# Performance work log

Measured on AMD Instinct MI355X. Metric: run time of the kernel, lower is better.

## Reference

```python
import jax, jax.numpy as jnp
import numpy as np


def _lstm(x, w_ih, w_hh, b_ih, b_hh):
    # x: [B, T, D]; w_ih: [4H, D]; w_hh: [4H, H]. PyTorch gate order: i, f, g, o.
    B, T, D = x.shape
    H = w_hh.shape[1]
    # Precompute input contributions for all timesteps: [B, T, 4H]
    xg = jnp.einsum('btd,gd->btg', x, w_ih) + b_ih + b_hh
    xg = jnp.transpose(xg, (1, 0, 2))  # [T, B, 4H]

    def step(carry, xt):
        h, c = carry
        gates = xt + h @ w_hh.T  # [B, 4H]
        i, f, g, o = jnp.split(gates, 4, axis=-1)
        i = jax.nn.sigmoid(i)
        f = jax.nn.sigmoid(f)
        g = jnp.tanh(g)
        o = jax.nn.sigmoid(o)
        c = f * c + i * g
        h = o * jnp.tanh(c)
        return (h, c), h

    h0 = jnp.zeros((B, H), dtype=x.dtype)
    c0 = jnp.zeros((B, H), dtype=x.dtype)
    (_, _), hs = jax.lax.scan(step, (h0, c0), xg)
    return jnp.transpose(hs, (1, 0, 2))  # [B, T, H]


def setup_inputs() -> dict:
    key = jax.random.key(0)
    ks = jax.random.split(key, 11)
    B, T, D, H1, H2, OUT = 2048, 128, 128, 128, 64, 64
    s1 = 1.0 / np.sqrt(H1)
    s2 = 1.0 / np.sqrt(H2)
    return {
        'x': jax.random.normal(ks[0], (B, T, D), dtype=jnp.float32),
        'w_ih1': jax.random.uniform(ks[1], (4 * H1, D), jnp.float32, -s1, s1),
        'w_hh1': jax.random.uniform(ks[2], (4 * H1, H1), jnp.float32, -s1, s1),
        'b_ih1': jax.random.uniform(ks[3], (4 * H1,), jnp.float32, -s1, s1),
        'b_hh1': jax.random.uniform(ks[4], (4 * H1,), jnp.float32, -s1, s1),
        'w_ih2': jax.random.uniform(ks[5], (4 * H2, H1), jnp.float32, -s2, s2),
        'w_hh2': jax.random.uniform(ks[6], (4 * H2, H2), jnp.float32, -s2, s2),
        'b_ih2': jax.random.uniform(ks[7], (4 * H2,), jnp.float32, -s2, s2),
        'b_hh2': jax.random.uniform(ks[8], (4 * H2,), jnp.float32, -s2, s2),
        'w_dense': jax.random.uniform(ks[9], (OUT, H2), jnp.float32, -s2, s2),
        'b_dense': jax.random.uniform(ks[10], (OUT,), jnp.float32, -s2, s2),
    }


def reference(x, w_ih1, w_hh1, b_ih1, b_hh1, w_ih2, w_hh2, b_ih2, b_hh2, w_dense, b_dense):
    # Dropout is identity in eval mode.
    h = _lstm(x, w_ih1, w_hh1, b_ih1, b_hh1)          # [B, T, H1]
    h = _lstm(h, w_ih2, w_hh2, b_ih2, b_hh2)          # [B, T, H2]
    last = h[:, -1, :]                                 # [B, H2]
    return jax.nn.relu(last @ w_dense.T + b_dense)     # [B, 64]
```

## Files before the change

kernel.cpp:

```cpp
#include <hip/hip_runtime.h>
#include <hip/hip_bf16.h>

#define BB  2048
#define TT  128
#define DD  128
#define HH1 128
#define GG1 512
#define HH2 64
#define GG2 256
#define OO  64

typedef __attribute__((ext_vector_type(8))) short  short8;
typedef __attribute__((ext_vector_type(4))) float  floatx4;

#define PIN(x) asm volatile("" : "+v"(x))

#define OFF_WHH1 0
#define OFF_WIH1 131072
#define OFF_WIH2 262144
#define OFF_WHH2 327680
#define OFF_B1   360448
#define OFF_B2   362496
#define OFF_XBF  524288
#define OFF_H1S  67633152

#define L2E      1.44269504088896340736f
#define TWO_L2E  2.88539008177792681472f

__device__ __forceinline__ short f2bf(float f) {
  unsigned u = __float_as_uint(f);
  unsigned r = (u + 0x7FFFu + ((u >> 16) & 1u)) >> 16;
  return (short)r;
}
__device__ __forceinline__ float exp2_f(float x) {
  float r; asm("v_exp_f32 %0, %1" : "=v"(r) : "v"(x)); return r;
}
__device__ __forceinline__ float sigm2(float y) {
  return __builtin_amdgcn_rcpf(1.0f + exp2_f(y));
}
__device__ __forceinline__ float tanh2(float y) {
  return fmaf(-2.0f, __builtin_amdgcn_rcpf(1.0f + exp2_f(y)), 1.0f);
}

__device__ __forceinline__ void lds_barrier() {
  asm volatile("s_waitcnt lgkmcnt(0)" ::: "memory");
  __builtin_amdgcn_s_barrier();
  asm volatile("" ::: "memory");
}

__global__ void k_prep(const float* __restrict__ wih1, const float* __restrict__ whh1,
                       const float* __restrict__ bih1, const float* __restrict__ bhh1,
                       const float* __restrict__ wih2, const float* __restrict__ whh2,
                       const float* __restrict__ bih2, const float* __restrict__ bhh2,
                       char* __restrict__ ws) {
  short* WHH1 = (short*)(ws + OFF_WHH1);
  short* WIH1 = (short*)(ws + OFF_WIH1);
  short* WIH2 = (short*)(ws + OFF_WIH2);
  short* WHH2 = (short*)(ws + OFF_WHH2);
  float* B1 = (float*)(ws + OFF_B1);
  float* B2 = (float*)(ws + OFF_B2);
  int idx = blockIdx.x * blockDim.x + threadIdx.x;
  int stride = gridDim.x * blockDim.x;
  const float SCI = -L2E, SCG = TWO_L2E;
  for (int i = idx; i < GG1 * DD; i += stride) {
    int g = (i >> 7) >> 7;
    float s = (g == 2) ? SCG : SCI;
    WIH1[i] = f2bf(wih1[i] * s); WHH1[i] = f2bf(whh1[i] * s);
  }
  for (int i = idx; i < GG2 * HH1; i += stride) {
    int g = (i >> 7) >> 6; float s = (g == 2) ? SCG : SCI;
    WIH2[i] = f2bf(wih2[i] * s);
  }
  for (int i = idx; i < GG2 * HH2; i += stride) {
    int g = (i >> 6) >> 6; float s = (g == 2) ? SCG : SCI;
    WHH2[i] = f2bf(whh2[i] * s);
  }
  for (int i = idx; i < GG1; i += stride) {
    float s = ((i >> 7) == 2) ? SCG : SCI;
    B1[i] = (bih1[i] + bhh1[i]) * s;
  }
  for (int i = idx; i < GG2; i += stride) {
    float s = ((i >> 6) == 2) ? SCG : SCI;
    B2[i] = (bih2[i] + bhh2[i]) * s;
  }
}

__global__ __launch_bounds__(256) void k_xcast(const float* __restrict__ x,
                                               short* __restrict__ xbf) {
  size_t i = ((size_t)blockIdx.x * 256 + threadIdx.x) * 8;
  float4 a = *(const float4*)&x[i];
  float4 b = *(const float4*)&x[i + 4];
  short8 o;
  o[0] = f2bf(a.x); o[1] = f2bf(a.y); o[2] = f2bf(a.z); o[3] = f2bf(a.w);
  o[4] = f2bf(b.x); o[5] = f2bf(b.y); o[6] = f2bf(b.z); o[7] = f2bf(b.w);
  *(short8*)&xbf[i] = o;
}

__global__ __launch_bounds__(512, 2) void k_rec1f(const char* __restrict__ ws,
                                                  short* __restrict__ h1s) {
  __shared__ short hbds[2][16 * 136];
  const short* WHH = (const short*)(ws + OFF_WHH1);
  const short* WIH = (const short*)(ws + OFF_WIH1);
  const short* XBF = (const short*)(ws + OFF_XBF);
  const float* B1 = (const float*)(ws + OFF_B1);
  const int lane = threadIdx.x & 63;
  const int wv = threadIdx.x >> 6;
  const int col = lane & 15, quad = lane >> 4;
  const int hc = wv * 16 + col;
  const int r0 = blockIdx.x * 8;

  short8 wh[4][4], wx[4][4];
#pragma unroll
  for (int gt = 0; gt < 4; ++gt)
#pragma unroll
    for (int kk = 0; kk < 4; ++kk) {
      wh[gt][kk] = *(const short8*)&WHH[(gt * 128 + hc) * HH1 + kk * 32 + quad * 8];
      wx[gt][kk] = *(const short8*)&WIH[(gt * 128 + hc) * DD + kk * 32 + quad * 8];
      PIN(wh[gt][kk]);
      PIN(wx[gt][kk]);
    }
  floatx4 BIASV[4];
#pragma unroll
  for (int gt = 0; gt < 4; ++gt) {
    float b = B1[gt * 128 + hc];
    BIASV[gt] = (floatx4){b, b, b, b};
    PIN(BIASV[gt]);
  }

  for (int i = threadIdx.x; i < 2 * 16 * 136; i += 512) ((short*)hbds)[i] = 0;

  const bool aload = (col < 8);
  const short* xbase = XBF + (size_t)(r0 + (col & 7)) * TT * DD;
  const short8 zz = {0, 0, 0, 0, 0, 0, 0, 0};
  short8 axA[4], axB[4];
  floatx4 accA[4], accB[4];

  {
    short8 ax0[4];
#pragma unroll
    for (int kk = 0; kk < 4; ++kk)
      ax0[kk] = aload ? *(const short8*)&xbase[kk * 32 + quad * 8] : zz;
#pragma unroll
    for (int gt = 0; gt < 4; ++gt)
      accA[gt] = __builtin_amdgcn_mfma_f32_16x16x32_bf16(ax0[0], wx[gt][0], BIASV[gt], 0, 0, 0);
#pragma unroll
    for (int kk = 1; kk < 4; ++kk)
#pragma unroll
      for (int gt = 0; gt < 4; ++gt)
        accA[gt] = __builtin_amdgcn_mfma_f32_16x16x32_bf16(ax0[kk], wx[gt][kk], accA[gt], 0, 0, 0);
  }
#pragma unroll
  for (int kk = 0; kk < 4; ++kk) {
    axA[kk] = aload ? *(const short8*)&xbase[DD + kk * 32 + quad * 8] : zz;
    axB[kk] = zz;
  }

  const int row0 = (quad & 1) * 4 + (quad >> 1) * 2;
  float c0 = 0.f, c1 = 0.f;
  __syncthreads();

  auto step = [&](int t, short* rbuf, short* wbuf, floatx4* A, floatx4* Bn,
                  short8* axC, short8* axP) {
    if (aload && t + 2 < TT) {
#pragma unroll
      for (int kk = 0; kk < 4; ++kk)
        axP[kk] = *(const short8*)&xbase[(t + 2) * DD + kk * 32 + quad * 8];
    }
    short8 ah[4];
#pragma unroll
    for (int kk = 0; kk < 4; ++kk)
      ah[kk] = *(const short8*)&rbuf[col * 136 + kk * 32 + quad * 8];
#pragma unroll
    for (int kk = 0; kk < 4; ++kk)
#pragma unroll
      for (int gt = 0; gt < 4; ++gt)
        A[gt] = __builtin_amdgcn_mfma_f32_16x16x32_bf16(ah[kk], wh[gt][kk], A[gt], 0, 0, 0);
#pragma unroll
    for (int gt = 0; gt < 4; ++gt)
      Bn[gt] = __builtin_amdgcn_mfma_f32_16x16x32_bf16(axC[0], wx[gt][0], BIASV[gt], 0, 0, 0);
#pragma unroll
    for (int kk = 1; kk < 4; ++kk)
#pragma unroll
      for (int gt = 0; gt < 4; ++gt)
        Bn[gt] = __builtin_amdgcn_mfma_f32_16x16x32_bf16(axC[kk], wx[gt][kk], Bn[gt], 0, 0, 0);

    float g0[4], g1[4];
#pragma unroll
    for (int gt = 0; gt < 4; ++gt) {
      float v2 = __shfl_xor(A[gt][2], 32);
      float v3 = __shfl_xor(A[gt][3], 32);
      g0[gt] = (quad < 2) ? A[gt][0] : v2;
      g1[gt] = (quad < 2) ? A[gt][1] : v3;
    }
    {
      float i0 = sigm2(g0[0]), f0 = sigm2(g0[1]), gg0 = tanh2(g0[2]), o0 = sigm2(g0[3]);
      c0 = fmaf(f0, c0, i0 * gg0);
      float hA = o0 * tanh2(c0 * TWO_L2E);
      float i1 = sigm2(g1[0]), f1 = sigm2(g1[1]), gg1 = tanh2(g1[2]), o1 = sigm2(g1[3]);
      c1 = fmaf(f1, c1, i1 * gg1);
      float hB = o1 * tanh2(c1 * TWO_L2E);
      short ha = f2bf(hA), hbv = f2bf(hB);
      wbuf[(row0)     * 136 + hc] = ha;
      wbuf[(row0 + 1) * 136 + hc] = hbv;
      h1s[((size_t)(r0 + row0)     * TT + t) * HH1 + hc] = ha;
      h1s[((size_t)(r0 + row0 + 1) * TT + t) * HH1 + hc] = hbv;
    }
    lds_barrier();
  };

  for (int t = 0; t < TT; t += 2) {
    step(t,     &hbds[0][0], &hbds[1][0], accA, accB, axA, axB);
    step(t + 1, &hbds[1][0], &hbds[0][0], accB, accA, axB, axA);
  }
}

__global__ __launch_bounds__(512, 2) void k_rec2w(const char* __restrict__ ws,
                                                  const short* __restrict__ h1s,
                                                  const float* __restrict__ wd,
                                                  const float* __restrict__ bd,
                                                  float* __restrict__ out) {
  __shared__ __align__(16) float xacc[2][256 * 20];
  __shared__ short hbuf[2][16 * 72];
  __shared__ float h2f[8 * HH2];
  const int lane = threadIdx.x & 63;
  const int wv = threadIdx.x >> 6;
  const int col = lane & 15, quad = lane >> 4;
  const int r0 = blockIdx.x * 8;

  for (int i = threadIdx.x; i < 2 * 256 * 20; i += 512) ((float*)xacc)[i] = 0.f;
  for (int i = threadIdx.x; i < 2 * 16 * 72; i += 512) ((short*)hbuf)[i] = 0;

  if (wv >= 4) {
    const short* WIH = (const short*)(ws + OFF_WIH2);
    const float* B2 = (const float*)(ws + OFF_B2);
    const int hcp = (wv - 4) * 16 + col;
    short8 wx[4][4];
#pragma unroll
    for (int gt = 0; gt < 4; ++gt)
#pragma unroll
      for (int kk = 0; kk < 4; ++kk) {
        wx[gt][kk] = *(const short8*)&WIH[(gt * 64 + hcp) * HH1 + kk * 32 + quad * 8];
        PIN(wx[gt][kk]);
      }
    floatx4 BIASV[4];
#pragma unroll
    for (int gt = 0; gt < 4; ++gt) {
      float b = B2[gt * 64 + hcp];
      BIASV[gt] = (floatx4){b, b, b, b};
      PIN(BIASV[gt]);
    }
    const bool aload = (col < 8);
    const short* h1base = h1s + (size_t)(r0 + (col & 7)) * TT * HH1;
    const short8 zz = {0, 0, 0, 0, 0, 0, 0, 0};
    short8 axA[4], axB[4];

    {
      short8 ax0[4];
#pragma unroll
      for (int kk = 0; kk < 4; ++kk)
        ax0[kk] = aload ? *(const short8*)&h1base[kk * 32 + quad * 8] : zz;
      floatx4 Bn[4];
#pragma unroll
      for (int gt = 0; gt < 4; ++gt)
        Bn[gt] = __builtin_amdgcn_mfma_f32_16x16x32_bf16(ax0[0], wx[gt][0], BIASV[gt], 0, 0, 0);
#pragma unroll
      for (int kk = 1; kk < 4; ++kk)
#pragma unroll
        for (int gt = 0; gt < 4; ++gt)
          Bn[gt] = __builtin_amdgcn_mfma_f32_16x16x32_bf16(ax0[kk], wx[gt][kk], Bn[gt], 0, 0, 0);
      if (quad < 2) {
#pragma unroll
        for (int gt = 0; gt < 4; ++gt)
          *(floatx4*)&xacc[0][(gt * 64 + hcp) * 20 + quad * 4] = Bn[gt];
      }
    }
#pragma unroll
    for (int kk = 0; kk < 4; ++kk) {
      axA[kk] = aload ? *(const short8*)&h1base[HH1 + kk * 32 + quad * 8] : zz;
      axB[kk] = zz;
    }
    __syncthreads();

    auto pstep = [&](int t, short8* axC, short8* axP) {
      if (t + 1 < TT) {
        floatx4 Bn[4];
#pragma unroll
        for (int gt = 0; gt < 4; ++gt)
          Bn[gt] = __builtin_amdgcn_mfma_f32_16x16x32_bf16(axC[0], wx[gt][0], BIASV[gt], 0, 0, 0);
#pragma unroll
        for (int kk = 1; kk < 4; ++kk)
#pragma unroll
          for (int gt = 0; gt < 4; ++gt)
            Bn[gt] = __builtin_amdgcn_mfma_f32_16x16x32_bf16(axC[kk], wx[gt][kk], Bn[gt], 0, 0, 0);
        if (quad < 2) {
#pragma unroll
          for (int gt = 0; gt < 4; ++gt)
            *(floatx4*)&xacc[(t + 1) & 1][(gt * 64 + hcp) * 20 + quad * 4] = Bn[gt];
        }
      }
      if (aload && t + 2 < TT) {
#pragma unroll
        for (int kk = 0; kk < 4; ++kk)
          axP[kk] = *(const short8*)&h1base[(t + 2) * HH1 + kk * 32 + quad * 8];
      }
      lds_barrier();
    };

    for (int t = 0; t < TT; t += 2) {
      pstep(t, axA, axB);
      pstep(t + 1, axB, axA);
    }

  } else {
    const short* WHH = (const short*)(ws + OFF_WHH2);
    const int hc = wv * 16 + col;
    short8 wh[4][2];
#pragma unroll
    for (int gt = 0; gt < 4; ++gt)
#pragma unroll
      for (int kk = 0; kk < 2; ++kk) {
        wh[gt][kk] = *(const short8*)&WHH[(gt * 64 + hc) * HH2 + kk * 32 + quad * 8];
        PIN(wh[gt][kk]);
      }
    const int row0 = (quad & 1) * 4 + (quad >> 1) * 2;
    float c0 = 0.f, c1 = 0.f;
    __syncthreads();

    auto cstep = [&](int t) {
      const int cur = t & 1;
      short8 ah[2];
#pragma unroll
      for (int kk = 0; kk < 2; ++kk)
        ah[kk] = *(const short8*)&hbuf[cur][col * 72 + kk * 32 + quad * 8];
      floatx4 A[4];
#pragma unroll
      for (int gt = 0; gt < 4; ++gt)
        A[gt] = *(const floatx4*)&xacc[cur][(gt * 64 + hc) * 20 + quad * 4];
#pragma unroll
      for (int kk = 0; kk < 2; ++kk)
#pragma unroll
        for (int gt = 0; gt < 4; ++gt)
          A[gt] = __builtin_amdgcn_mfma_f32_16x16x32_bf16(ah[kk], wh[gt][kk], A[gt], 0, 0, 0);

      float g0[4], g1[4];
#pragma unroll
      for (int gt = 0; gt < 4; ++gt) {
        float v2 = __shfl_xor(A[gt][2], 32);
        float v3 = __shfl_xor(A[gt][3], 32);
        g0[gt] = (quad < 2) ? A[gt][0] : v2;
        g1[gt] = (quad < 2) ? A[gt][1] : v3;
      }
      float i0 = sigm2(g0[0]), f0 = sigm2(g0[1]), gg0 = tanh2(g0[2]), o0 = sigm2(g0[3]);
      c0 = fmaf(f0, c0, i0 * gg0);
      float hA = o0 * tanh2(c0 * TWO_L2E);
      float i1 = sigm2(g1[0]), f1 = sigm2(g1[1]), gg1 = tanh2(g1[2]), o1 = sigm2(g1[3]);
      c1 = fmaf(f1, c1, i1 * gg1);
      float hB = o1 * tanh2(c1 * TWO_L2E);
      hbuf[cur ^ 1][(row0)     * 72 + hc] = f2bf(hA);
      hbuf[cur ^ 1][(row0 + 1) * 72 + hc] = f2bf(hB);
      if (t == TT - 1) {
        h2f[(row0)     * HH2 + hc] = hA;
        h2f[(row0 + 1) * HH2 + hc] = hB;
      }
      lds_barrier();
    };

    for (int t = 0; t < TT; ++t) cstep(t);
  }

  __syncthreads();

  {
    const int o = threadIdx.x & 63;
    const int r = threadIdx.x >> 6;
    float acc = bd[o];
    for (int k = 0; k < HH2; ++k)
      acc = fmaf(h2f[r * HH2 + k], wd[o * HH2 + k], acc);
    out[(size_t)(r0 + r) * OO + o] = fmaxf(acc, 0.f);
  }
}

extern "C" void kernel_launch(void* const* d_in, const int* in_sizes, int n_in,
                              void* d_out, int out_size, void* d_ws, size_t ws_size,
                              hipStream_t stream) {
  const float* x       = (const float*)d_in[0];
  const float* w_ih1   = (const float*)d_in[1];
  const float* w_hh1   = (const float*)d_in[2];
  const float* b_ih1   = (const float*)d_in[3];
  const float* b_hh1   = (const float*)d_in[4];
  const float* w_ih2   = (const float*)d_in[5];
  const float* w_hh2   = (const float*)d_in[6];
  const float* b_ih2   = (const float*)d_in[7];
  const float* b_hh2   = (const float*)d_in[8];
  const float* w_dense = (const float*)d_in[9];
  const float* b_dense = (const float*)d_in[10];
  char* ws = (char*)d_ws;
  short* xbf = (short*)(ws + OFF_XBF);
  short* h1s = (short*)(ws + OFF_H1S);
  float* out = (float*)d_out;

  hipLaunchKernelGGL(k_prep, dim3(256), dim3(256), 0, stream,
                     w_ih1, w_hh1, b_ih1, b_hh1, w_ih2, w_hh2, b_ih2, b_hh2, ws);
  hipLaunchKernelGGL(k_xcast, dim3((BB * TT * DD) / (256 * 8)), dim3(256), 0, stream, x, xbf);
  hipLaunchKernelGGL(k_rec1f, dim3(BB / 8), dim3(512), 0, stream, ws, h1s);
  hipLaunchKernelGGL(k_rec2w, dim3(BB / 8), dim3(512), 0, stream, ws, h1s, w_dense, b_dense, out);
}
```

Measured before the change: 414.4 us.

## Fuse x bf16 cast into layer-1 recurrence via LDS ring buffer

Removes the separate x-to-bf16 cast kernel. The layer-1 recurrent kernel now reads fp32 x directly, converts it with packed bf16 conversion, and stages it into a 4-deep LDS ring with register prefetch several timesteps ahead. This eliminates a full write and reread of the bf16 copy of x and one kernel launch. In exchange, the recurrent kernel does the conversion and the larger fp32 loads, and uses extra LDS.

```diff
diff --git a/kernel.cpp b/kernel.cpp
--- a/kernel.cpp
+++ b/kernel.cpp
@@ -21,7 +21,6 @@
 #define OFF_WHH2 327680
 #define OFF_B1   360448
 #define OFF_B2   362496
-#define OFF_XBF  524288
 #define OFF_H1S  67633152
 
 #define L2E      1.44269504088896340736f
@@ -40,6 +39,11 @@
 }
 __device__ __forceinline__ float tanh2(float y) {
   return fmaf(-2.0f, __builtin_amdgcn_rcpf(1.0f + exp2_f(y)), 1.0f);
+}
+__device__ __forceinline__ unsigned cvtpk(float a, float b) {
+  unsigned r;
+  asm("v_cvt_pk_bf16_f32 %0, %1, %2" : "=v"(r) : "v"(a), "v"(b));
+  return r;
 }
 
 __device__ __forceinline__ void lds_barrier() {
@@ -85,23 +89,13 @@
   }
 }
 
-__global__ __launch_bounds__(256) void k_xcast(const float* __restrict__ x,
-                                               short* __restrict__ xbf) {
-  size_t i = ((size_t)blockIdx.x * 256 + threadIdx.x) * 8;
-  float4 a = *(const float4*)&x[i];
-  float4 b = *(const float4*)&x[i + 4];
-  short8 o;
-  o[0] = f2bf(a.x); o[1] = f2bf(a.y); o[2] = f2bf(a.z); o[3] = f2bf(a.w);
-  o[4] = f2bf(b.x); o[5] = f2bf(b.y); o[6] = f2bf(b.z); o[7] = f2bf(b.w);
-  *(short8*)&xbf[i] = o;
-}
-
 __global__ __launch_bounds__(512, 2) void k_rec1f(const char* __restrict__ ws,
+                                                  const float* __restrict__ x,
                                                   short* __restrict__ h1s) {
   __shared__ short hbds[2][16 * 136];
+  __shared__ short ring[4][8 * 136];
   const short* WHH = (const short*)(ws + OFF_WHH1);
   const short* WIH = (const short*)(ws + OFF_WIH1);
-  const short* XBF = (const short*)(ws + OFF_XBF);
   const float* B1 = (const float*)(ws + OFF_B1);
   const int lane = threadIdx.x & 63;
   const int wv = threadIdx.x >> 6;
@@ -129,8 +123,20 @@
 
   for (int i = threadIdx.x; i < 2 * 16 * 136; i += 512) ((short*)hbds)[i] = 0;
 
+  const int rrow = threadIdx.x >> 6;
+  const int rcp  = threadIdx.x & 63;
+  const float* xsrc = x + (size_t)(r0 + rrow) * TT * DD + rcp * 2;
+
+#pragma unroll
+  for (int tt = 0; tt < 4; ++tt) {
+    float2 f = *(const float2*)&xsrc[tt * DD];
+    *(unsigned*)&ring[tt][rrow * 136 + rcp * 2] = cvtpk(f.x, f.y);
+  }
+  float2 pfA = *(const float2*)&xsrc[4 * DD];
+  float2 pfB = pfA;
+  __syncthreads();
+
   const bool aload = (col < 8);
-  const short* xbase = XBF + (size_t)(r0 + (col & 7)) * TT * DD;
   const short8 zz = {0, 0, 0, 0, 0, 0, 0, 0};
   short8 axA[4], axB[4];
   floatx4 accA[4], accB[4];
@@ -139,7 +145,7 @@
     short8 ax0[4];
 #pragma unroll
     for (int kk = 0; kk < 4; ++kk)
-      ax0[kk] = aload ? *(const short8*)&xbase[kk * 32 + quad * 8] : zz;
+      ax0[kk] = aload ? *(const short8*)&ring[0][col * 136 + kk * 32 + quad * 8] : zz;
 #pragma unroll
     for (int gt = 0; gt < 4; ++gt)
       accA[gt] = __builtin_amdgcn_mfma_f32_16x16x32_bf16(ax0[0], wx[gt][0], BIASV[gt], 0, 0, 0);
@@ -151,20 +157,24 @@
   }
 #pragma unroll
   for (int kk = 0; kk < 4; ++kk) {
-    axA[kk] = aload ? *(const short8*)&xbase[DD + kk * 32 + quad * 8] : zz;
+    axA[kk] = aload ? *(const short8*)&ring[1][col * 136 + kk * 32 + quad * 8] : zz;
     axB[kk] = zz;
   }
+  __syncthreads();
 
   const int row0 = (quad & 1) * 4 + (quad >> 1) * 2;
   float c0 = 0.f, c1 = 0.f;
-  __syncthreads();
 
   auto step = [&](int t, short* rbuf, short* wbuf, floatx4* A, floatx4* Bn,
-                  short8* axC, short8* axP) {
+                  short8* axC, short8* axP, float2& pfC, float2& pfP) {
+    if (t + 4 < TT)
+      *(unsigned*)&ring[t & 3][rrow * 136 + rcp * 2] = cvtpk(pfC.x, pfC.y);
+    if (t + 5 < TT)
+      pfP = *(const float2*)&xsrc[(t + 5) * DD];
     if (aload && t + 2 < TT) {
 #pragma unroll
       for (int kk = 0; kk < 4; ++kk)
-        axP[kk] = *(const short8*)&xbase[(t + 2) * DD + kk * 32 + quad * 8];
+        axP[kk] = *(const short8*)&ring[(t + 2) & 3][col * 136 + kk * 32 + quad * 8];
     }
     short8 ah[4];
 #pragma unroll
@@ -209,8 +219,8 @@
   };
 
   for (int t = 0; t < TT; t += 2) {
-    step(t,     &hbds[0][0], &hbds[1][0], accA, accB, axA, axB);
-    step(t + 1, &hbds[1][0], &hbds[0][0], accB, accA, axB, axA);
+    step(t,     &hbds[0][0], &hbds[1][0], accA, accB, axA, axB, pfA, pfB);
+    step(t + 1, &hbds[1][0], &hbds[0][0], accB, accA, axB, axA, pfB, pfA);
   }
 }
 
@@ -395,13 +405,11 @@
   const float* w_dense = (const float*)d_in[9];
   const float* b_dense = (const float*)d_in[10];
   char* ws = (char*)d_ws;
-  short* xbf = (short*)(ws + OFF_XBF);
   short* h1s = (short*)(ws + OFF_H1S);
   float* out = (float*)d_out;
 
   hipLaunchKernelGGL(k_prep, dim3(256), dim3(256), 0, stream,
                      w_ih1, w_hh1, b_ih1, b_hh1, w_ih2, w_hh2, b_ih2, b_hh2, ws);
-  hipLaunchKernelGGL(k_xcast, dim3((BB * TT * DD) / (256 * 8)), dim3(256), 0, stream, x, xbf);
-  hipLaunchKernelGGL(k_rec1f, dim3(BB / 8), dim3(512), 0, stream, ws, h1s);
+  hipLaunchKernelGGL(k_rec1f, dim3(BB / 8), dim3(512), 0, stream, ws, x, h1s);
   hipLaunchKernelGGL(k_rec2w, dim3(BB / 8), dim3(512), 0, stream, ws, h1s, w_dense, b_dense, out);
 }
```

After: 362.4 us. 12.6% less time.
